# Optimization experiments

Hardware: AMD Instinct MI355X
Metric: run time of the kernel (lower is better)

Reference implementation:

```python
import jax, jax.numpy as jnp
import numpy as np

N = 50000      # nodes
E = 800000     # edges (before self-loops)
F_IN = 128     # num_features
H = 4          # heads
C = 64         # hidden_channels
HC = H * C     # 256
NEG_SLOPE = 0.2


def setup_inputs() -> dict:
    key = jax.random.key(0)
    ks = jax.random.split(key, 20)
    x = jax.random.normal(ks[0], (N, F_IN), dtype=jnp.float32)
    edge_index = jax.random.randint(ks[1], (2, E), 0, N, dtype=jnp.int32)
    s = 0.05
    inp = {"x": x, "edge_index": edge_index}
    dims_in = [F_IN, HC, HC, HC]
    for l in range(4):
        kW, ka, kb = jax.random.split(ks[2 + l], 3)
        inp[f"W{l+1}"] = jax.random.normal(kW, (dims_in[l], HC), dtype=jnp.float32) * s
        inp[f"a_src{l+1}"] = jax.random.normal(ka, (H, C), dtype=jnp.float32) * s
        inp[f"a_dst{l+1}"] = jax.random.normal(kb, (H, C), dtype=jnp.float32) * s
        inp[f"b{l+1}"] = jnp.zeros((HC,), dtype=jnp.float32)
    return inp


def gat_conv(x, src, dst, W, a_src, a_dst, b):
    # x: [N, F_in] -> h: [N, H, C]
    h = (x @ W).reshape(N, H, C)
    es = jnp.sum(h * a_src, axis=-1)  # [N, H] per-node source logits
    ed = jnp.sum(h * a_dst, axis=-1)  # [N, H]
    e = jax.nn.leaky_relu(es[src] + ed[dst], NEG_SLOPE)  # [Etot, H]
    m = jax.ops.segment_max(e, dst, num_segments=N)      # per-dst max
    m = jnp.where(jnp.isfinite(m), m, 0.0)
    ex = jnp.exp(e - m[dst])
    denom = jax.ops.segment_sum(ex, dst, num_segments=N)
    alpha = ex / (denom[dst] + 1e-16)                     # edge softmax
    out = jax.ops.segment_sum(alpha[:, :, None] * h[src], dst, num_segments=N)
    return out.reshape(N, HC) + b


def reference(x, edge_index,
              W1, a_src1, a_dst1, b1,
              W2, a_src2, a_dst2, b2,
              W3, a_src3, a_dst3, b3,
              W4, a_src4, a_dst4, b4):
    loop = jnp.arange(N, dtype=edge_index.dtype)
    src = jnp.concatenate([edge_index[0], loop])  # add self-loops (PyG default)
    dst = jnp.concatenate([edge_index[1], loop])
    x1 = jax.nn.relu(gat_conv(x, src, dst, W1, a_src1, a_dst1, b1))
    x2 = jax.nn.relu(gat_conv(x1, src, dst, W2, a_src2, a_dst2, b2))
    x3 = jax.nn.relu(gat_conv(x2 + x1, src, dst, W3, a_src3, a_dst3, b3))
    x4 = jax.nn.relu(gat_conv(x2 + x3, src, dst, W4, a_src4, a_dst4, b4))
    # NOTE: source code calls conv4 again (not conv5) -- reproduced faithfully
    x5 = gat_conv(x4 + x3, src, dst, W4, a_src4, a_dst4, b4)
    return x5
```

## Files before the change

kernel.cpp:

```cpp
#include <hip/hip_runtime.h>
#include <hip/hip_bf16.h>

#define N_NODES 50000
#define E_EDGES 800000
#define ETOT (E_EDGES + N_NODES)
#define HC 256
#define NHEAD 4
#define CHAN 64
#define NEG 0.2f
#define NBLK ((N_NODES + 1023) / 1024)

typedef _Float16 half8 __attribute__((ext_vector_type(8)));
typedef _Float16 half4v __attribute__((ext_vector_type(4)));
typedef float float4v __attribute__((ext_vector_type(4)));


__global__ void count_kernel(const int* __restrict__ ei, int* __restrict__ counts) {
    int i = blockIdx.x * blockDim.x + threadIdx.x;
    if (i >= ETOT) return;
    int dst = (i < E_EDGES) ? ei[E_EDGES + i] : (i - E_EDGES);
    atomicAdd(&counts[dst], 1);
}

__global__ __launch_bounds__(256) void blocksum_kernel(const int* __restrict__ counts,
                                                       int* __restrict__ blocksums) {
    __shared__ int s[4];
    int b = blockIdx.x, tid = threadIdx.x;
    int base = b * 1024;
    int sum = 0;
    #pragma unroll
    for (int r = 0; r < 4; ++r) {
        int idx = base + r * 256 + tid;
        sum += (idx < N_NODES) ? counts[idx] : 0;
    }
    #pragma unroll
    for (int m = 1; m < 64; m <<= 1) sum += __shfl_xor(sum, m, 64);
    if ((tid & 63) == 0) s[tid >> 6] = sum;
    __syncthreads();
    if (tid == 0) blocksums[b] = s[0] + s[1] + s[2] + s[3];
}

__global__ __launch_bounds__(64) void blockscan_kernel(int* __restrict__ blocksums) {
    int tid = threadIdx.x;
    int v = (tid < NBLK) ? blocksums[tid] : 0;
    #pragma unroll
    for (int off = 1; off < 64; off <<= 1) {
        int t = __shfl_up(v, off, 64);
        if (tid >= off) v += t;
    }
    if (tid < NBLK) blocksums[tid] = v;
}

__global__ __launch_bounds__(1024) void scatter_scan_kernel(const int* __restrict__ counts,
                                                            const int* __restrict__ blocksums,
                                                            int* __restrict__ offsets,
                                                            int* __restrict__ cursor) {
    __shared__ int s[1024];
    int b = blockIdx.x, tid = threadIdx.x;
    int idx = b * 1024 + tid;
    int v = (idx < N_NODES) ? counts[idx] : 0;
    s[tid] = v;
    __syncthreads();
    for (int off = 1; off < 1024; off <<= 1) {
        int t = (tid >= off) ? s[tid - off] : 0;
        __syncthreads();
        s[tid] += t;
        __syncthreads();
    }
    int excl = s[tid] - v + (b > 0 ? blocksums[b - 1] : 0);
    if (idx < N_NODES) { offsets[idx] = excl; cursor[idx] = excl; }
    if (idx == N_NODES - 1) offsets[N_NODES] = excl + v;
}

__global__ void fill_kernel(const int* __restrict__ ei, int* __restrict__ cursor,
                            int* __restrict__ csr_src, int* __restrict__ csr_dst) {
    int i = blockIdx.x * blockDim.x + threadIdx.x;
    if (i >= ETOT) return;
    int src, dst;
    if (i < E_EDGES) { src = ei[i]; dst = ei[E_EDGES + i]; }
    else             { src = i - E_EDGES; dst = src; }
    int pos = atomicAdd(&cursor[dst], 1);
    csr_src[pos] = src;
    csr_dst[pos] = dst;
}


__global__ void wsplit_kernel(const float* __restrict__ W, _Float16* __restrict__ Wth,
                              _Float16* __restrict__ Wtl, int K) {
    int id = blockIdx.x * 256 + threadIdx.x;
    if (id >= K * 256) return;
    int n = id & 255, k = id >> 8;
    float w = W[(size_t)k * 256 + n];
    _Float16 h = (_Float16)w;
    _Float16 l = (_Float16)(w - (float)h);
    Wth[(size_t)n * K + k] = h;
    Wtl[(size_t)n * K + k] = l;
}

__global__ void xsplit_kernel(const float* __restrict__ x, _Float16* __restrict__ xh,
                              _Float16* __restrict__ xl, int total) {
    int id = blockIdx.x * 256 + threadIdx.x;
    if (id >= total) return;
    float v = x[id];
    _Float16 h = (_Float16)v;
    xh[id] = h;
    xl[id] = (_Float16)(v - (float)h);
}


__global__ __launch_bounds__(256) void edge_alpha_kernel(
        const float* __restrict__ es, const float* __restrict__ ed,
        const int* __restrict__ csr_src, const int* __restrict__ csr_dst,
        float* __restrict__ ex) {
    int e = blockIdx.x * 256 + threadIdx.x;
    if (e >= ETOT) return;
    int s = csr_src[e], d = csr_dst[e];
    float4 esv = *(const float4*)(es + (size_t)s * 4);
    float4 edv = *(const float4*)(ed + (size_t)d * 4);
    float4 v;
    v.x = esv.x + edv.x; v.y = esv.y + edv.y;
    v.z = esv.z + edv.z; v.w = esv.w + edv.w;
    v.x = (v.x > 0.f) ? v.x : NEG * v.x;
    v.y = (v.y > 0.f) ? v.y : NEG * v.y;
    v.z = (v.z > 0.f) ? v.z : NEG * v.z;
    v.w = (v.w > 0.f) ? v.w : NEG * v.w;
    v.x = __expf(v.x); v.y = __expf(v.y);
    v.z = __expf(v.z); v.w = __expf(v.w);
    *(float4*)(ex + (size_t)e * 4) = v;
}


template<int K, bool HASLO>
struct SmemLayout {
    _Float16 Ah[64][K + 8];
    _Float16 Al[HASLO ? 64 : 1][HASLO ? (K + 8) : 8];
    _Float16 Bh[256][40];
    _Float16 Bl[256][40];
};
template<int K, bool HASLO>
union SmemU {
    SmemLayout<K, HASLO> t;
    _Float16 out[64][264];
};

template<int K, bool HASLO, bool HAS2>
__global__ __launch_bounds__(256) void gemm_mfma_kernel(
        const _Float16* __restrict__ A1h, const _Float16* __restrict__ A1l,
        const _Float16* __restrict__ A2h,
        const _Float16* __restrict__ Wth, const _Float16* __restrict__ Wtl,
        const float* __restrict__ a_src, const float* __restrict__ a_dst,
        _Float16* __restrict__ H16, float* __restrict__ es, float* __restrict__ ed,
        int M) {
    constexpr int NC  = K / 32;
    constexpr int CPR = K / 8;
    __shared__ SmemU<K, HASLO> u;
    auto& Ah = u.t.Ah;
    auto& Al = u.t.Al;
    auto& Bh = u.t.Bh;
    auto& Bl = u.t.Bl;

    int tid = threadIdx.x;
    int m0 = blockIdx.x * 64;
    int w = tid >> 6, lane = tid & 63;
    int rn = w * 64;
    int fr = lane & 15;
    int q  = lane >> 4;
    int fk = q * 8;

    int wr = tid >> 2;
    int wk = (tid & 3) * 8;

    half8 a1c[NC], a2c[HAS2 ? NC : 1], alc[HASLO ? NC : 1];
    #pragma unroll
    for (int c = 0; c < NC; ++c) {
        int idx = c * 256 + tid;
        int row = idx / CPR, col = (idx % CPR) * 8;
        int grow = m0 + row;
        a1c[c] = (half8)(_Float16)0;
        if (grow < M) a1c[c] = *(const half8*)(A1h + (size_t)grow * K + col);
        if constexpr (HAS2) {
            a2c[c] = (half8)(_Float16)0;
            if (grow < M) a2c[c] = *(const half8*)(A2h + (size_t)grow * K + col);
        }
        if constexpr (HASLO) {
            alc[c] = (half8)(_Float16)0;
            if (grow < M) alc[c] = *(const half8*)(A1l + (size_t)grow * K + col);
        }
    }
    half8 pbh[4], pbl[4];
    auto loadB = [&](int k0) {
        #pragma unroll
        for (int g = 0; g < 4; ++g) {
            int r = g * 64 + wr;
            pbh[g] = *(const half8*)(Wth + (size_t)r * K + k0 + wk);
            pbl[g] = *(const half8*)(Wtl + (size_t)r * K + k0 + wk);
        }
    };
    loadB(0);

    #pragma unroll
    for (int c = 0; c < NC; ++c) {
        int idx = c * 256 + tid;
        int row = idx / CPR, col = (idx % CPR) * 8;
        half8 v = a1c[c];
        if constexpr (HAS2) v = v + a2c[c];
        *(half8*)&Ah[row][col] = v;
        if constexpr (HASLO) *(half8*)&Al[row][col] = alc[c];
    }

    float4v acc[4][4];
    #pragma unroll
    for (int i = 0; i < 4; ++i)
        #pragma unroll
        for (int j = 0; j < 4; ++j)
            acc[i][j] = (float4v){0.f, 0.f, 0.f, 0.f};

    __syncthreads();

    for (int kk = 0; kk < K / 32; ++kk) {
        int k0 = kk * 32;
        #pragma unroll
        for (int g = 0; g < 4; ++g) {
            int r = g * 64 + wr;
            *(half8*)&Bh[r][wk] = pbh[g];
            *(half8*)&Bl[r][wk] = pbl[g];
        }
        __syncthreads();
        if (kk + 1 < K / 32) loadB(k0 + 32);
        half8 afh[4], bfh[4], bfl[4];
        #pragma unroll
        for (int t = 0; t < 4; ++t) {
            afh[t] = *(const half8*)&Ah[t * 16 + fr][k0 + fk];
            bfh[t] = *(const half8*)&Bh[rn + t * 16 + fr][fk];
            bfl[t] = *(const half8*)&Bl[rn + t * 16 + fr][fk];
        }
        if constexpr (HASLO) {
            half8 afl[4];
            #pragma unroll
            for (int t = 0; t < 4; ++t) afl[t] = *(const half8*)&Al[t * 16 + fr][k0 + fk];
            #pragma unroll
            for (int tm = 0; tm < 4; ++tm)
                #pragma unroll
                for (int tn = 0; tn < 4; ++tn)
                    acc[tm][tn] = __builtin_amdgcn_mfma_f32_16x16x32_f16(
                        afl[tm], bfh[tn], acc[tm][tn], 0, 0, 0);
        }
        #pragma unroll
        for (int tm = 0; tm < 4; ++tm)
            #pragma unroll
            for (int tn = 0; tn < 4; ++tn) {
                float4v c = acc[tm][tn];
                c = __builtin_amdgcn_mfma_f32_16x16x32_f16(afh[tm], bfl[tn], c, 0, 0, 0);
                c = __builtin_amdgcn_mfma_f32_16x16x32_f16(afh[tm], bfh[tn], c, 0, 0, 0);
                acc[tm][tn] = c;
            }
        __syncthreads();
    }

    float asv[4], adv[4];
    #pragma unroll
    for (int tn = 0; tn < 4; ++tn) {
        asv[tn] = a_src[w * CHAN + tn * 16 + fr];
        adv[tn] = a_dst[w * CHAN + tn * 16 + fr];
    }
    #pragma unroll
    for (int tm = 0; tm < 4; ++tm) {
        #pragma unroll
        for (int i = 0; i < 4; ++i) {
            int r = tm * 16 + q * 4 + i;
            float ps = 0.f, pd = 0.f;
            #pragma unroll
            for (int tn = 0; tn < 4; ++tn) {
                float hv = acc[tm][tn][i];
                ps += hv * asv[tn];
                pd += hv * adv[tn];
                u.out[r][rn + tn * 16 + fr] = (_Float16)hv;
            }
            #pragma unroll
            for (int msk = 1; msk < 16; msk <<= 1) {
                ps += __shfl_xor(ps, msk, 64);
                pd += __shfl_xor(pd, msk, 64);
            }
            int row = m0 + r;
            if (fr == 0 && row < M) {
                es[row * NHEAD + w] = ps;
                ed[row * NHEAD + w] = pd;
            }
        }
    }
    __syncthreads();

    #pragma unroll
    for (int k = 0; k < 8; ++k) {
        int c = k * 256 + tid;
        int r = c >> 5, cc = c & 31;
        if (m0 + r < M) {
            half8 v = *(const half8*)(&u.out[r][0] + cc * 8);
            *(half8*)(H16 + (size_t)(m0 + r) * HC + cc * 8) = v;
        }
    }
}


__global__ __launch_bounds__(256) void gat_aggregate_kernel(
        const _Float16* __restrict__ H16, const float* __restrict__ ex,
        const int* __restrict__ offsets, const int* __restrict__ csr_src,
        const float* __restrict__ bias, _Float16* __restrict__ out16,
        float* __restrict__ out32, int do_relu, int node_base) {
    __shared__ float ex_lds[4][256];
    __shared__ int   src_lds[4][64];
    int tid = threadIdx.x;
    int w = tid >> 6, lane = tid & 63;
    int n = node_base + blockIdx.x * 4 + w;
    int off = offsets[n];
    int deg = offsets[n + 1] - off;

    if (deg <= 64) {
        int sreg = n;
        float4 ex4 = make_float4(0.f, 0.f, 0.f, 0.f);
        if (lane < deg) {
            sreg = csr_src[off + lane];
            ex4 = *(const float4*)(ex + (size_t)(off + lane) * 4);
        }
        src_lds[w][lane] = sreg;
        *(float4*)&ex_lds[w][lane * 4] = ex4;

        int hl = lane & 31, side = lane >> 5;
        int hd = hl >> 3;
        float av[8] = {0.f, 0.f, 0.f, 0.f, 0.f, 0.f, 0.f, 0.f};
        int degr = (deg + 7) & ~7;
        #pragma unroll 2
        for (int j0 = 0; j0 < degr; j0 += 8) {
            int j = j0 + side;
            int s0 = src_lds[w][j];
            int s1 = src_lds[w][j + 2];
            int s2 = src_lds[w][j + 4];
            int s3 = src_lds[w][j + 6];
            float w0 = ex_lds[w][j * 4 + hd];
            float w1 = ex_lds[w][(j + 2) * 4 + hd];
            float w2 = ex_lds[w][(j + 4) * 4 + hd];
            float w3 = ex_lds[w][(j + 6) * 4 + hd];
            half8 h0 = *(const half8*)(H16 + (size_t)s0 * HC + hl * 8);
            half8 h1 = *(const half8*)(H16 + (size_t)s1 * HC + hl * 8);
            half8 h2 = *(const half8*)(H16 + (size_t)s2 * HC + hl * 8);
            half8 h3 = *(const half8*)(H16 + (size_t)s3 * HC + hl * 8);
            #pragma unroll
            for (int c = 0; c < 8; ++c) {
                av[c] += w0 * (float)h0[c];
                av[c] += w1 * (float)h1[c];
                av[c] += w2 * (float)h2[c];
                av[c] += w3 * (float)h3[c];
            }
        }

        float4 l4 = ex4;
        #pragma unroll
        for (int msk = 1; msk < 64; msk <<= 1) {
            l4.x += __shfl_xor(l4.x, msk, 64);
            l4.y += __shfl_xor(l4.y, msk, 64);
            l4.z += __shfl_xor(l4.z, msk, 64);
            l4.w += __shfl_xor(l4.w, msk, 64);
        }
        #pragma unroll
        for (int c = 0; c < 8; ++c) av[c] += __shfl_xor(av[c], 32, 64);
        if (side == 0) {
            float denom = (hd == 0) ? l4.x : (hd == 1) ? l4.y : (hd == 2) ? l4.z : l4.w;
            float scale = 1.f / (denom + 1e-16f);
            float4 b0 = *(const float4*)(bias + hl * 8);
            float4 b1 = *(const float4*)(bias + hl * 8 + 4);
            float o[8] = {av[0] * scale + b0.x, av[1] * scale + b0.y,
                          av[2] * scale + b0.z, av[3] * scale + b0.w,
                          av[4] * scale + b1.x, av[5] * scale + b1.y,
                          av[6] * scale + b1.z, av[7] * scale + b1.w};
            if (do_relu)
                #pragma unroll
                for (int c = 0; c < 8; ++c) o[c] = fmaxf(o[c], 0.f);
            if (out16) {
                half8 ov = {(_Float16)o[0], (_Float16)o[1], (_Float16)o[2], (_Float16)o[3],
                            (_Float16)o[4], (_Float16)o[5], (_Float16)o[6], (_Float16)o[7]};
                *(half8*)(out16 + (size_t)n * HC + hl * 8) = ov;
            } else {
                *(float4*)(out32 + (size_t)n * HC + hl * 8) =
                    make_float4(o[0], o[1], o[2], o[3]);
                *(float4*)(out32 + (size_t)n * HC + hl * 8 + 4) =
                    make_float4(o[4], o[5], o[6], o[7]);
            }
        }
        return;
    }

    int head = lane >> 4;
    float4 acc0 = make_float4(0.f, 0.f, 0.f, 0.f);
    float den = 0.f;
    for (int j = 0; j < deg; ++j) {
        int s = csr_src[off + j];
        float exv = ex[(size_t)(off + j) * 4 + head];
        den += exv;
        half4v h0 = *(const half4v*)(H16 + (size_t)s * HC + lane * 4);
        acc0.x += exv * (float)h0[0]; acc0.y += exv * (float)h0[1];
        acc0.z += exv * (float)h0[2]; acc0.w += exv * (float)h0[3];
    }
    float scale = 1.f / (den + 1e-16f);
    float4 b4 = *(const float4*)(bias + lane * 4);
    float o[4] = {acc0.x * scale + b4.x, acc0.y * scale + b4.y,
                  acc0.z * scale + b4.z, acc0.w * scale + b4.w};
    if (do_relu)
        #pragma unroll
        for (int c = 0; c < 4; ++c) o[c] = fmaxf(o[c], 0.f);
    if (out16) {
        half4v ov = {(_Float16)o[0], (_Float16)o[1], (_Float16)o[2], (_Float16)o[3]};
        *(half4v*)(out16 + (size_t)n * HC + lane * 4) = ov;
    } else {
        *(float4*)(out32 + (size_t)n * HC + lane * 4) = make_float4(o[0], o[1], o[2], o[3]);
    }
}


extern "C" void kernel_launch(void* const* d_in, const int* in_sizes, int n_in,
                              void* d_out, int out_size, void* d_ws, size_t ws_size,
                              hipStream_t stream) {
    const float* x  = (const float*)d_in[0];
    const int*   ei = (const int*)d_in[1];
    const float *W[5], *Asrc[5], *Adst[5], *Bs[5];
    for (int l = 0; l < 4; ++l) {
        W[l]    = (const float*)d_in[2 + l * 4];
        Asrc[l] = (const float*)d_in[3 + l * 4];
        Adst[l] = (const float*)d_in[4 + l * 4];
        Bs[l]   = (const float*)d_in[5 + l * 4];
    }
    W[4] = W[3]; Asrc[4] = Asrc[3]; Adst[4] = Adst[3]; Bs[4] = Bs[3];

    char* ws = (char*)d_ws;
    size_t off = 0;
    auto alloc = [&](size_t bytes) -> void* {
        void* p = ws + off;
        off += (bytes + 255) & ~(size_t)255;
        return p;
    };
    _Float16* h16  = (_Float16*)alloc((size_t)N_NODES * HC * 2);
    _Float16* xa   = (_Float16*)alloc((size_t)N_NODES * HC * 2);
    _Float16* xb   = (_Float16*)alloc((size_t)N_NODES * HC * 2);
    _Float16* xc   = (_Float16*)alloc((size_t)N_NODES * HC * 2);
    _Float16* xd   = (_Float16*)alloc((size_t)N_NODES * HC * 2);
    _Float16* xh   = (_Float16*)alloc((size_t)N_NODES * 128 * 2);
    _Float16* xl   = (_Float16*)alloc((size_t)N_NODES * 128 * 2);
    float* es      = (float*)alloc((size_t)N_NODES * 4 * 4);
    float* ed      = (float*)alloc((size_t)N_NODES * 4 * 4);
    float* exbuf   = (float*)alloc((size_t)ETOT * 4 * 4);
    int*   counts  = (int*)alloc((size_t)N_NODES * 4);
    int*   offsets = (int*)alloc((size_t)(N_NODES + 1) * 4);
    int*   cursor  = (int*)alloc((size_t)N_NODES * 4);
    int*   csr_src = (int*)alloc((size_t)ETOT * 4);
    int*   csr_dst = (int*)alloc((size_t)ETOT * 4);
    int*   blocksums = (int*)alloc((size_t)NBLK * 4);
    _Float16 *Wth[5], *Wtl[5];
    int Ks[4] = {128, 256, 256, 256};
    for (int l = 0; l < 4; ++l) {
        Wth[l] = (_Float16*)alloc((size_t)256 * Ks[l] * 2);
        Wtl[l] = (_Float16*)alloc((size_t)256 * Ks[l] * 2);
    }
    Wth[4] = Wth[3]; Wtl[4] = Wtl[3];

    hipMemsetAsync(counts, 0, (size_t)N_NODES * 4, stream);
    count_kernel<<<(ETOT + 255) / 256, 256, 0, stream>>>(ei, counts);
    blocksum_kernel<<<NBLK, 256, 0, stream>>>(counts, blocksums);
    blockscan_kernel<<<1, 64, 0, stream>>>(blocksums);
    scatter_scan_kernel<<<NBLK, 1024, 0, stream>>>(counts, blocksums, offsets, cursor);
    fill_kernel<<<(ETOT + 255) / 256, 256, 0, stream>>>(ei, cursor, csr_src, csr_dst);
    for (int l = 0; l < 4; ++l)
        wsplit_kernel<<<(Ks[l] * 256 + 255) / 256, 256, 0, stream>>>(W[l], Wth[l], Wtl[l], Ks[l]);
    xsplit_kernel<<<(N_NODES * 128 + 255) / 256, 256, 0, stream>>>(x, xh, xl, N_NODES * 128);

    int gemm_grid = (N_NODES + 63) / 64;
    auto agg = [&](int l, _Float16* o16, float* o32, int relu) {
        edge_alpha_kernel<<<(ETOT + 255) / 256, 256, 0, stream>>>(
            es, ed, csr_src, csr_dst, exbuf);
        gat_aggregate_kernel<<<N_NODES / 8, 256, 0, stream>>>(
            h16, exbuf, offsets, csr_src, Bs[l], o16, o32, relu, 0);
        gat_aggregate_kernel<<<N_NODES / 8, 256, 0, stream>>>(
            h16, exbuf, offsets, csr_src, Bs[l], o16, o32, relu, N_NODES / 2);
    };

    float* out = (float*)d_out;
    gemm_mfma_kernel<128, true, false><<<gemm_grid, 256, 0, stream>>>(
        xh, xl, nullptr, Wth[0], Wtl[0], Asrc[0], Adst[0], h16, es, ed, N_NODES);
    agg(0, xa, nullptr, 1);
    gemm_mfma_kernel<256, false, false><<<gemm_grid, 256, 0, stream>>>(
        xa, nullptr, nullptr, Wth[1], Wtl[1], Asrc[1], Adst[1], h16, es, ed, N_NODES);
    agg(1, xb, nullptr, 1);
    gemm_mfma_kernel<256, false, true><<<gemm_grid, 256, 0, stream>>>(
        xb, nullptr, xa, Wth[2], Wtl[2], Asrc[2], Adst[2], h16, es, ed, N_NODES);
    agg(2, xc, nullptr, 1);
    gemm_mfma_kernel<256, false, true><<<gemm_grid, 256, 0, stream>>>(
        xb, nullptr, xc, Wth[3], Wtl[3], Asrc[3], Adst[3], h16, es, ed, N_NODES);
    agg(3, xd, nullptr, 1);
    gemm_mfma_kernel<256, false, true><<<gemm_grid, 256, 0, stream>>>(
        xd, nullptr, xc, Wth[4], Wtl[4], Asrc[4], Adst[4], h16, es, ed, N_NODES);
    agg(4, nullptr, out, 0);
}
```

Baseline: 770.0 us.

## Make aggregation persistent with next-node prefetch and interleave CSR src/dst

The aggregation kernel becomes a grid-stride persistent kernel over a fixed number of blocks. Each wave prefetches the next node's offsets, neighbour indices and edge weights while it aggregates the current node, which hides gather latency, and the two half-grid launches become a single launch. The CSR src and dst arrays are interleaved into one int2 array, so the edge-weight kernel does a single 8-byte load per edge. In exchange, the neighbour-index reads in aggregation now load 8 bytes to use 4, and the persistent loop depends on the chosen grid size and a launch-bounds occupancy hint.

Measured after the change: 1.344 ms. +74.6%, slower.

```diff
diff --git a/kernel.cpp b/kernel.cpp
--- a/kernel.cpp
+++ b/kernel.cpp
@@ -9,6 +9,7 @@
 #define CHAN 64
 #define NEG 0.2f
 #define NBLK ((N_NODES + 1023) / 1024)
+#define AGG_BLOCKS 2048
 
 typedef _Float16 half8 __attribute__((ext_vector_type(8)));
 typedef _Float16 half4v __attribute__((ext_vector_type(4)));
@@ -73,15 +74,14 @@
 }
 
 __global__ void fill_kernel(const int* __restrict__ ei, int* __restrict__ cursor,
-                            int* __restrict__ csr_src, int* __restrict__ csr_dst) {
+                            int2* __restrict__ csr) {
     int i = blockIdx.x * blockDim.x + threadIdx.x;
     if (i >= ETOT) return;
     int src, dst;
     if (i < E_EDGES) { src = ei[i]; dst = ei[E_EDGES + i]; }
     else             { src = i - E_EDGES; dst = src; }
     int pos = atomicAdd(&cursor[dst], 1);
-    csr_src[pos] = src;
-    csr_dst[pos] = dst;
+    csr[pos] = make_int2(src, dst);
 }
 
 
@@ -110,13 +110,12 @@
 
 __global__ __launch_bounds__(256) void edge_alpha_kernel(
         const float* __restrict__ es, const float* __restrict__ ed,
-        const int* __restrict__ csr_src, const int* __restrict__ csr_dst,
-        float* __restrict__ ex) {
+        const int2* __restrict__ csr, float* __restrict__ ex) {
     int e = blockIdx.x * 256 + threadIdx.x;
     if (e >= ETOT) return;
-    int s = csr_src[e], d = csr_dst[e];
-    float4 esv = *(const float4*)(es + (size_t)s * 4);
-    float4 edv = *(const float4*)(ed + (size_t)d * 4);
+    int2 sd = csr[e];
+    float4 esv = *(const float4*)(es + (size_t)sd.x * 4);
+    float4 edv = *(const float4*)(ed + (size_t)sd.y * 4);
     float4 v;
     v.x = esv.x + edv.x; v.y = esv.y + edv.y;
     v.z = esv.z + edv.z; v.w = esv.w + edv.w;
@@ -302,116 +301,141 @@
 }
 
 
-__global__ __launch_bounds__(256) void gat_aggregate_kernel(
+__global__ __launch_bounds__(256, 8) void gat_aggregate_kernel(
         const _Float16* __restrict__ H16, const float* __restrict__ ex,
-        const int* __restrict__ offsets, const int* __restrict__ csr_src,
+        const int* __restrict__ offsets, const int2* __restrict__ csr,
         const float* __restrict__ bias, _Float16* __restrict__ out16,
-        float* __restrict__ out32, int do_relu, int node_base) {
+        float* __restrict__ out32, int do_relu, int nwaves) {
     __shared__ float ex_lds[4][256];
     __shared__ int   src_lds[4][64];
     int tid = threadIdx.x;
     int w = tid >> 6, lane = tid & 63;
-    int n = node_base + blockIdx.x * 4 + w;
+    int hl = lane & 31, side = lane >> 5;
+    int hd = hl >> 3;
+
+    int n = blockIdx.x * 4 + w;
+    if (n >= N_NODES) return;
+
     int off = offsets[n];
     int deg = offsets[n + 1] - off;
-
-    if (deg <= 64) {
-        int sreg = n;
-        float4 ex4 = make_float4(0.f, 0.f, 0.f, 0.f);
-        if (lane < deg) {
-            sreg = csr_src[off + lane];
-            ex4 = *(const float4*)(ex + (size_t)(off + lane) * 4);
-        }
-        src_lds[w][lane] = sreg;
-        *(float4*)&ex_lds[w][lane * 4] = ex4;
-
-        int hl = lane & 31, side = lane >> 5;
-        int hd = hl >> 3;
-        float av[8] = {0.f, 0.f, 0.f, 0.f, 0.f, 0.f, 0.f, 0.f};
-        int degr = (deg + 7) & ~7;
-        #pragma unroll 2
-        for (int j0 = 0; j0 < degr; j0 += 8) {
-            int j = j0 + side;
-            int s0 = src_lds[w][j];
-            int s1 = src_lds[w][j + 2];
-            int s2 = src_lds[w][j + 4];
-            int s3 = src_lds[w][j + 6];
-            float w0 = ex_lds[w][j * 4 + hd];
-            float w1 = ex_lds[w][(j + 2) * 4 + hd];
-            float w2 = ex_lds[w][(j + 4) * 4 + hd];
-            float w3 = ex_lds[w][(j + 6) * 4 + hd];
-            half8 h0 = *(const half8*)(H16 + (size_t)s0 * HC + hl * 8);
-            half8 h1 = *(const half8*)(H16 + (size_t)s1 * HC + hl * 8);
-            half8 h2 = *(const half8*)(H16 + (size_t)s2 * HC + hl * 8);
-            half8 h3 = *(const half8*)(H16 + (size_t)s3 * HC + hl * 8);
-            #pragma unroll
-            for (int c = 0; c < 8; ++c) {
-                av[c] += w0 * (float)h0[c];
-                av[c] += w1 * (float)h1[c];
-                av[c] += w2 * (float)h2[c];
-                av[c] += w3 * (float)h3[c];
-            }
-        }
-
-        float4 l4 = ex4;
-        #pragma unroll
-        for (int msk = 1; msk < 64; msk <<= 1) {
-            l4.x += __shfl_xor(l4.x, msk, 64);
-            l4.y += __shfl_xor(l4.y, msk, 64);
-            l4.z += __shfl_xor(l4.z, msk, 64);
-            l4.w += __shfl_xor(l4.w, msk, 64);
-        }
-        #pragma unroll
-        for (int c = 0; c < 8; ++c) av[c] += __shfl_xor(av[c], 32, 64);
-        if (side == 0) {
-            float denom = (hd == 0) ? l4.x : (hd == 1) ? l4.y : (hd == 2) ? l4.z : l4.w;
-            float scale = 1.f / (denom + 1e-16f);
-            float4 b0 = *(const float4*)(bias + hl * 8);
-            float4 b1 = *(const float4*)(bias + hl * 8 + 4);
-            float o[8] = {av[0] * scale + b0.x, av[1] * scale + b0.y,
-                          av[2] * scale + b0.z, av[3] * scale + b0.w,
-                          av[4] * scale + b1.x, av[5] * scale + b1.y,
-                          av[6] * scale + b1.z, av[7] * scale + b1.w};
+    int sreg = n;
+    float4 ex4 = make_float4(0.f, 0.f, 0.f, 0.f);
+    if (deg <= 64 && lane < deg) {
+        sreg = csr[off + lane].x;
+        ex4 = *(const float4*)(ex + (size_t)(off + lane) * 4);
+    }
+
+    while (true) {
+        int cdeg = deg, coff = off, cn = n;
+        float4 cex = ex4;
+        if (cdeg <= 64) {
+            src_lds[w][lane] = sreg;
+            *(float4*)&ex_lds[w][lane * 4] = ex4;
+        }
+
+        int nn = n + nwaves;
+        bool have_next = (nn < N_NODES);
+        if (have_next) {
+            off = offsets[nn];
+            deg = offsets[nn + 1] - off;
+            sreg = nn;
+            ex4 = make_float4(0.f, 0.f, 0.f, 0.f);
+            if (deg <= 64 && lane < deg) {
+                sreg = csr[off + lane].x;
+                ex4 = *(const float4*)(ex + (size_t)(off + lane) * 4);
+            }
+        }
+
+        if (cdeg <= 64) {
+            float av[8] = {0.f, 0.f, 0.f, 0.f, 0.f, 0.f, 0.f, 0.f};
+            int degr = (cdeg + 7) & ~7;
+            #pragma unroll 2
+            for (int j0 = 0; j0 < degr; j0 += 8) {
+                int j = j0 + side;
+                int s0 = src_lds[w][j];
+                int s1 = src_lds[w][j + 2];
+                int s2 = src_lds[w][j + 4];
+                int s3 = src_lds[w][j + 6];
+                float w0 = ex_lds[w][j * 4 + hd];
+                float w1 = ex_lds[w][(j + 2) * 4 + hd];
+                float w2 = ex_lds[w][(j + 4) * 4 + hd];
+                float w3 = ex_lds[w][(j + 6) * 4 + hd];
+                half8 h0 = *(const half8*)(H16 + (size_t)s0 * HC + hl * 8);
+                half8 h1 = *(const half8*)(H16 + (size_t)s1 * HC + hl * 8);
+                half8 h2 = *(const half8*)(H16 + (size_t)s2 * HC + hl * 8);
+                half8 h3 = *(const half8*)(H16 + (size_t)s3 * HC + hl * 8);
+                #pragma unroll
+                for (int c = 0; c < 8; ++c) {
+                    av[c] += w0 * (float)h0[c];
+                    av[c] += w1 * (float)h1[c];
+                    av[c] += w2 * (float)h2[c];
+                    av[c] += w3 * (float)h3[c];
+                }
+            }
+
+            float4 l4 = cex;
+            #pragma unroll
+            for (int msk = 1; msk < 64; msk <<= 1) {
+                l4.x += __shfl_xor(l4.x, msk, 64);
+                l4.y += __shfl_xor(l4.y, msk, 64);
+                l4.z += __shfl_xor(l4.z, msk, 64);
+                l4.w += __shfl_xor(l4.w, msk, 64);
+            }
+            #pragma unroll
+            for (int c = 0; c < 8; ++c) av[c] += __shfl_xor(av[c], 32, 64);
+            if (side == 0) {
+                float denom = (hd == 0) ? l4.x : (hd == 1) ? l4.y : (hd == 2) ? l4.z : l4.w;
+                float scale = 1.f / (denom + 1e-16f);
+                float4 b0 = *(const float4*)(bias + hl * 8);
+                float4 b1 = *(const float4*)(bias + hl * 8 + 4);
+                float o[8] = {av[0] * scale + b0.x, av[1] * scale + b0.y,
+                              av[2] * scale + b0.z, av[3] * scale + b0.w,
+                              av[4] * scale + b1.x, av[5] * scale + b1.y,
+                              av[6] * scale + b1.z, av[7] * scale + b1.w};
+                if (do_relu)
+                    #pragma unroll
+                    for (int c = 0; c < 8; ++c) o[c] = fmaxf(o[c], 0.f);
+                if (out16) {
+                    half8 ov = {(_Float16)o[0], (_Float16)o[1], (_Float16)o[2], (_Float16)o[3],
+                                (_Float16)o[4], (_Float16)o[5], (_Float16)o[6], (_Float16)o[7]};
+                    *(half8*)(out16 + (size_t)cn * HC + hl * 8) = ov;
+                } else {
+                    *(float4*)(out32 + (size_t)cn * HC + hl * 8) =
+                        make_float4(o[0], o[1], o[2], o[3]);
+                    *(float4*)(out32 + (size_t)cn * HC + hl * 8 + 4) =
+                        make_float4(o[4], o[5], o[6], o[7]);
+                }
+            }
+        } else {
+            int head = lane >> 4;
+            float4 acc0 = make_float4(0.f, 0.f, 0.f, 0.f);
+            float den = 0.f;
+            for (int j = 0; j < cdeg; ++j) {
+                int s = csr[coff + j].x;
+                float exv = ex[(size_t)(coff + j) * 4 + head];
+                den += exv;
+                half4v h0 = *(const half4v*)(H16 + (size_t)s * HC + lane * 4);
+                acc0.x += exv * (float)h0[0]; acc0.y += exv * (float)h0[1];
+                acc0.z += exv * (float)h0[2]; acc0.w += exv * (float)h0[3];
+            }
+            float scale = 1.f / (den + 1e-16f);
+            float4 b4 = *(const float4*)(bias + lane * 4);
+            float o[4] = {acc0.x * scale + b4.x, acc0.y * scale + b4.y,
+                          acc0.z * scale + b4.z, acc0.w * scale + b4.w};
             if (do_relu)
                 #pragma unroll
-                for (int c = 0; c < 8; ++c) o[c] = fmaxf(o[c], 0.f);
+                for (int c = 0; c < 4; ++c) o[c] = fmaxf(o[c], 0.f);
             if (out16) {
-                half8 ov = {(_Float16)o[0], (_Float16)o[1], (_Float16)o[2], (_Float16)o[3],
-                            (_Float16)o[4], (_Float16)o[5], (_Float16)o[6], (_Float16)o[7]};
-                *(half8*)(out16 + (size_t)n * HC + hl * 8) = ov;
+                half4v ov = {(_Float16)o[0], (_Float16)o[1], (_Float16)o[2], (_Float16)o[3]};
+                *(half4v*)(out16 + (size_t)cn * HC + lane * 4) = ov;
             } else {
-                *(float4*)(out32 + (size_t)n * HC + hl * 8) =
+                *(float4*)(out32 + (size_t)cn * HC + lane * 4) =
                     make_float4(o[0], o[1], o[2], o[3]);
-                *(float4*)(out32 + (size_t)n * HC + hl * 8 + 4) =
-                    make_float4(o[4], o[5], o[6], o[7]);
-            }
-        }
-        return;
-    }
-
-    int head = lane >> 4;
-    float4 acc0 = make_float4(0.f, 0.f, 0.f, 0.f);
-    float den = 0.f;
-    for (int j = 0; j < deg; ++j) {
-        int s = csr_src[off + j];
-        float exv = ex[(size_t)(off + j) * 4 + head];
-        den += exv;
-        half4v h0 = *(const half4v*)(H16 + (size_t)s * HC + lane * 4);
-        acc0.x += exv * (float)h0[0]; acc0.y += exv * (float)h0[1];
-        acc0.z += exv * (float)h0[2]; acc0.w += exv * (float)h0[3];
-    }
-    float scale = 1.f / (den + 1e-16f);
-    float4 b4 = *(const float4*)(bias + lane * 4);
-    float o[4] = {acc0.x * scale + b4.x, acc0.y * scale + b4.y,
-                  acc0.z * scale + b4.z, acc0.w * scale + b4.w};
-    if (do_relu)
-        #pragma unroll
-        for (int c = 0; c < 4; ++c) o[c] = fmaxf(o[c], 0.f);
-    if (out16) {
-        half4v ov = {(_Float16)o[0], (_Float16)o[1], (_Float16)o[2], (_Float16)o[3]};
-        *(half4v*)(out16 + (size_t)n * HC + lane * 4) = ov;
-    } else {
-        *(float4*)(out32 + (size_t)n * HC + lane * 4) = make_float4(o[0], o[1], o[2], o[3]);
+            }
+        }
+
+        if (!have_next) break;
+        n = nn;
     }
 }
 
@@ -450,8 +474,7 @@
     int*   counts  = (int*)alloc((size_t)N_NODES * 4);
     int*   offsets = (int*)alloc((size_t)(N_NODES + 1) * 4);
     int*   cursor  = (int*)alloc((size_t)N_NODES * 4);
-    int*   csr_src = (int*)alloc((size_t)ETOT * 4);
-    int*   csr_dst = (int*)alloc((size_t)ETOT * 4);
+    int2*  csr     = (int2*)alloc((size_t)ETOT * 8);
     int*   blocksums = (int*)alloc((size_t)NBLK * 4);
     _Float16 *Wth[5], *Wtl[5];
     int Ks[4] = {128, 256, 256, 256};
@@ -466,7 +489,7 @@
     blocksum_kernel<<<NBLK, 256, 0, stream>>>(counts, blocksums);
     blockscan_kernel<<<1, 64, 0, stream>>>(blocksums);
     scatter_scan_kernel<<<NBLK, 1024, 0, stream>>>(counts, blocksums, offsets, cursor);
-    fill_kernel<<<(ETOT + 255) / 256, 256, 0, stream>>>(ei, cursor, csr_src, csr_dst);
+    fill_kernel<<<(ETOT + 255) / 256, 256, 0, stream>>>(ei, cursor, csr);
     for (int l = 0; l < 4; ++l)
         wsplit_kernel<<<(Ks[l] * 256 + 255) / 256, 256, 0, stream>>>(W[l], Wth[l], Wtl[l], Ks[l]);
     xsplit_kernel<<<(N_NODES * 128 + 255) / 256, 256, 0, stream>>>(x, xh, xl, N_NODES * 128);
@@ -474,11 +497,9 @@
     int gemm_grid = (N_NODES + 63) / 64;
     auto agg = [&](int l, _Float16* o16, float* o32, int relu) {
         edge_alpha_kernel<<<(ETOT + 255) / 256, 256, 0, stream>>>(
-            es, ed, csr_src, csr_dst, exbuf);
-        gat_aggregate_kernel<<<N_NODES / 8, 256, 0, stream>>>(
-            h16, exbuf, offsets, csr_src, Bs[l], o16, o32, relu, 0);
-        gat_aggregate_kernel<<<N_NODES / 8, 256, 0, stream>>>(
-            h16, exbuf, offsets, csr_src, Bs[l], o16, o32, relu, N_NODES / 2);
+            es, ed, csr, exbuf);
+        gat_aggregate_kernel<<<AGG_BLOCKS, 256, 0, stream>>>(
+            h16, exbuf, offsets, csr, Bs[l], o16, o32, relu, AGG_BLOCKS * 4);
     };
 
     float* out = (float*)d_out;
```
